# Optimization experiments

Measured on AMD Instinct MI355X. Metric: run time of the kernel, lower is better.

Reference implementation:

```python
import jax, jax.numpy as jnp
import numpy as np
from functools import partial

N_NODES = 50000
N_EDGES = 1600000
D_IN, D_HID, D_OUT = 128, 128, 64


def gcn_layer(h, src, dst, w, W, b, act):
    # linear
    h = h @ W.T + b  # [N, d_out]
    n = h.shape[0]
    # degree with self-loop: rowsum = 1 + sum_{e: src=i} w_e (coalesce is linear, so dup-sum is implicit)
    deg = 1.0 + jax.ops.segment_sum(w, src, num_segments=n)
    d_inv = jnp.where(deg > 0, deg ** -0.5, 0.0)  # deg >= 1 so never inf; matches torch isinf->0
    # normalized SpMM: self-loop term + neighbor aggregation
    ew = d_inv[src] * w * d_inv[dst]  # [E]
    agg = jax.ops.segment_sum(ew[:, None] * h[dst], src, num_segments=n)  # [N, d_out]
    out = (d_inv ** 2)[:, None] * h + agg
    if act:
        out = jax.nn.relu(out)
    return out


def setup_inputs() -> dict:
    key = jax.random.key(0)
    ks = jax.random.split(key, 9)
    x = jax.random.normal(ks[0], (N_NODES, D_IN), dtype=jnp.float32)
    edge_index = jax.random.randint(ks[1], (2, N_EDGES), 0, N_NODES, dtype=jnp.int64)
    edge_weight = jnp.ones((N_EDGES,), dtype=jnp.float32)
    def xavier(k, fan_out, fan_in, gain=jnp.sqrt(2.0)):
        std = gain * jnp.sqrt(2.0 / (fan_in + fan_out))
        return (std * jax.random.normal(k, (fan_out, fan_in))).astype(jnp.float32)
    W1 = xavier(ks[2], D_HID, D_IN); b1 = jnp.zeros((D_HID,), jnp.float32)
    W2 = xavier(ks[3], D_HID, D_HID); b2 = jnp.zeros((D_HID,), jnp.float32)
    W3 = xavier(ks[4], D_OUT, D_HID); b3 = jnp.zeros((D_OUT,), jnp.float32)
    return {"x": x, "edge_index": edge_index, "edge_weight": edge_weight,
            "W1": W1, "b1": b1, "W2": W2, "b2": b2, "W3": W3, "b3": b3}


def reference(x, edge_index, edge_weight, W1, b1, W2, b2, W3, b3):
    src, dst = edge_index[0], edge_index[1]
    h = gcn_layer(x, src, dst, edge_weight, W1, b1, act=True)
    h = gcn_layer(h, src, dst, edge_weight, W2, b2, act=True)
    h = gcn_layer(h, src, dst, edge_weight, W3, b3, act=False)
    return h
```

## Files before the change

kernel.cpp:

```cpp
#include <hip/hip_runtime.h>


#define THREADS 256
#define CAP 72

typedef unsigned short bfu;

static inline int ceil_div(int a, int b) { return (a + b - 1) / b; }
static inline size_t alignup(size_t x) { return (x + 255) & ~(size_t)255; }


__global__ void k_zero(int* __restrict__ flag) {
  if (threadIdx.x == 0 && blockIdx.x == 0) { flag[0] = 0; flag[1] = 0; }
}


__global__ void k_init(int* __restrict__ counts, int n,
                       const int* __restrict__ ei_words,
                       const float* __restrict__ w, int e,
                       int* __restrict__ flag) {
  int i = blockIdx.x * blockDim.x + threadIdx.x;
  if (i < n) counts[i] = 0;
  if (i == 0) {
    int is64 = 1;
    for (int k = 0; k < 64; ++k) {
      if (ei_words[2 * k + 1] != 0) { is64 = 0; break; }
    }
    if (is64) flag[0] = 1;
  }
  if (i < e) {
    if (w[i] != 1.0f) atomicExch(&flag[1], 1);
  }
}

__device__ __forceinline__ int load_idx(const void* base, long long i, int is64) {
  if (is64) return (int)((const long long*)base)[i];
  return ((const int*)base)[i];
}


__global__ void k_count(const void* __restrict__ ei, int* __restrict__ counts,
                        int e, const int* __restrict__ flag) {
  int i = blockIdx.x * blockDim.x + threadIdx.x;
  if (i < e) {
    int is64 = flag[0];
    int s = load_idx(ei, i, is64);
    atomicAdd(&counts[s], 1);
  }
}


#define SCAN_T 256
#define SCAN_ITEMS 8
#define SCAN_BLOCK (SCAN_T * SCAN_ITEMS)

__global__ void k_scan1(const int* __restrict__ counts, int* __restrict__ row_ptr1,
                        int* __restrict__ partials, int n) {
  __shared__ int sd[SCAN_T];
  int t = threadIdx.x;
  int base = blockIdx.x * SCAN_BLOCK + t * SCAN_ITEMS;
  int v[SCAN_ITEMS];
  int s = 0;
#pragma unroll
  for (int i = 0; i < SCAN_ITEMS; ++i) {
    int idx = base + i;
    v[i] = (idx < n) ? counts[idx] : 0;
    s += v[i];
  }
  sd[t] = s;
  __syncthreads();
  for (int off = 1; off < SCAN_T; off <<= 1) {
    int x = 0;
    if (t >= off) x = sd[t - off];
    __syncthreads();
    sd[t] += x;
    __syncthreads();
  }
  int run = (t > 0) ? sd[t - 1] : 0;
  if (t == SCAN_T - 1) partials[blockIdx.x] = sd[t];
#pragma unroll
  for (int i = 0; i < SCAN_ITEMS; ++i) {
    run += v[i];
    int idx = base + i;
    if (idx < n) row_ptr1[idx] = run;
  }
}

__global__ void k_scan2(int* __restrict__ partials, int nb) {
  if (blockIdx.x == 0 && threadIdx.x == 0) {
    int run = 0;
    for (int b = 0; b < nb; ++b) {
      int v = partials[b];
      partials[b] = run;
      run += v;
    }
  }
}

__global__ void k_scan3(int* __restrict__ row_ptr, const int* __restrict__ partials,
                        int* __restrict__ cursor, int n) {
  int i = blockIdx.x * blockDim.x + threadIdx.x;
  if (i < n) {
    int b = i / SCAN_BLOCK;
    int v = row_ptr[i + 1] + partials[b];
    row_ptr[i + 1] = v;
    if (i + 1 < n) cursor[i + 1] = v;
  }
  if (i == 0) { row_ptr[0] = 0; cursor[0] = 0; }
}


__global__ void k_fill(const void* __restrict__ ei, const float* __restrict__ w,
                       int* __restrict__ cur, int* __restrict__ eg, int e,
                       const int* __restrict__ flag, int use_ell) {
  int i = blockIdx.x * blockDim.x + threadIdx.x;
  if (i >= e) return;
  int is64 = flag[0];
  int wnot1 = flag[1];
  int s = load_idx(ei, i, is64);
  int d = load_idx(ei, (long long)e + i, is64);
  int r = atomicAdd(&cur[s], 1);
  int p;
  if (use_ell) {
    if (r >= CAP) return;
    p = s * CAP + r;
  } else {
    p = r;
  }
  if (wnot1) {
    ((int2*)eg)[p] = make_int2(d, __float_as_int(w[i]));
  } else {
    eg[p] = d;
  }
}


__global__ void k_deg_w1(const int* __restrict__ cnt, const int* __restrict__ rp,
                         float* __restrict__ dinv, int n,
                         const int* __restrict__ flag, int use_ell) {
  if (flag[1] != 0) return;
  int i = blockIdx.x * blockDim.x + threadIdx.x;
  if (i >= n) return;
  int len = use_ell ? min(cnt[i], CAP) : (rp[i + 1] - rp[i]);
  float d = 1.0f + (float)len;
  dinv[i] = 1.0f / sqrtf(d);
}


__global__ __launch_bounds__(256) void k_deg_gen(const int* __restrict__ eg,
                                                 const int* __restrict__ cnt,
                                                 const int* __restrict__ rp,
                                                 float* __restrict__ dinv, int n,
                                                 const int* __restrict__ flag,
                                                 int use_ell) {
  if (flag[1] == 0) return;
  constexpr int G = 16;
  int node = blockIdx.x * (256 / G) + threadIdx.x / G;
  int l = threadIdx.x & (G - 1);
  if (node >= n) return;
  const int2* eg2 = (const int2*)eg;
  int e0, e1;
  if (use_ell) { e0 = node * CAP; e1 = e0 + min(cnt[node], CAP); }
  else { e0 = rp[node]; e1 = rp[node + 1]; }
  float s = 0.f;
  for (int e = e0 + l; e < e1; e += G) s += __int_as_float(eg2[e].y);
  s += __shfl_xor(s, 8);
  s += __shfl_xor(s, 4);
  s += __shfl_xor(s, 2);
  s += __shfl_xor(s, 1);
  if (l == 0) {
    float d = 1.0f + s;
    dinv[node] = (d > 0.0f) ? (1.0f / sqrtf(d)) : 0.0f;
  }
}


__global__ __launch_bounds__(256) void k_scale(int* __restrict__ eg,
                                               const int* __restrict__ cnt,
                                               const int* __restrict__ rp,
                                               const float* __restrict__ dinv, int n,
                                               const int* __restrict__ flag,
                                               int use_ell) {
  if (flag[1] == 0) return;
  constexpr int G = 16;
  int node = blockIdx.x * (256 / G) + threadIdx.x / G;
  int l = threadIdx.x & (G - 1);
  if (node >= n) return;
  int2* eg2 = (int2*)eg;
  float ds = dinv[node];
  int e0, e1;
  if (use_ell) { e0 = node * CAP; e1 = e0 + min(cnt[node], CAP); }
  else { e0 = rp[node]; e1 = rp[node + 1]; }
  for (int e = e0 + l; e < e1; e += G) {
    int2 ed = eg2[e];
    float v = ds * __int_as_float(ed.y) * dinv[ed.x];
    eg2[e] = make_int2(ed.x, __float_as_int(v));
  }
}


__device__ __forceinline__ bfu f2bf(float f) {
  unsigned u = __float_as_uint(f);
  unsigned r = (u + 0x7fffu + ((u >> 16) & 1u)) >> 16;
  return (bfu)r;
}


__global__ __launch_bounds__(256) void k_gemm(const float* __restrict__ A,
                                              const float* __restrict__ W,
                                              const float* __restrict__ bias,
                                              bfu* __restrict__ O, int M, int Nc) {
  __shared__ float4 xs[64][17];
  __shared__ float4 wsm[64][17];
  int tid = threadIdx.x;
  int m0 = blockIdx.x * 64;
  int c0 = blockIdx.y * 64;
  int tx = tid & 15, ty = tid >> 4;

  const float4* A4 = (const float4*)A;
  const float4* W4 = (const float4*)W;

  int r0 = tid >> 4;
  int k40 = tid & 15;

  float acc[4][4];
#pragma unroll
  for (int i = 0; i < 4; ++i)
#pragma unroll
    for (int j = 0; j < 4; ++j) acc[i][j] = 0.f;

  for (int ks = 0; ks < 2; ++ks) {
    if (ks) __syncthreads();
#pragma unroll
    for (int f = 0; f < 4; ++f) {
      int r = r0 + 16 * f;
      int gr = m0 + r;
      xs[r][k40] = (gr < M) ? A4[(size_t)gr * 32 + ks * 16 + k40]
                            : make_float4(0.f, 0.f, 0.f, 0.f);
      int wr = c0 + r;
      wsm[r][k40] = (wr < Nc) ? W4[(size_t)wr * 32 + ks * 16 + k40]
                              : make_float4(0.f, 0.f, 0.f, 0.f);
    }
    __syncthreads();

#pragma unroll
    for (int k4 = 0; k4 < 16; ++k4) {
      float4 a[4], b[4];
#pragma unroll
      for (int i = 0; i < 4; ++i) a[i] = xs[ty + 16 * i][k4];
#pragma unroll
      for (int j = 0; j < 4; ++j) b[j] = wsm[tx + 16 * j][k4];
#pragma unroll
      for (int i = 0; i < 4; ++i)
#pragma unroll
        for (int j = 0; j < 4; ++j) {
          acc[i][j] = fmaf(a[i].x, b[j].x, acc[i][j]);
          acc[i][j] = fmaf(a[i].y, b[j].y, acc[i][j]);
          acc[i][j] = fmaf(a[i].z, b[j].z, acc[i][j]);
          acc[i][j] = fmaf(a[i].w, b[j].w, acc[i][j]);
        }
    }
  }

#pragma unroll
  for (int i = 0; i < 4; ++i) {
    int r = m0 + ty + 16 * i;
    if (r < M) {
#pragma unroll
      for (int j = 0; j < 4; ++j) {
        int c = c0 + tx + 16 * j;
        O[(size_t)r * Nc + c] = f2bf(acc[i][j] + bias[c]);
      }
    }
  }
}


#define FMA8(v, u, acc)                                                       \
  do {                                                                        \
    acc[0] = fmaf((v), __uint_as_float((u).x << 16), acc[0]);                 \
    acc[1] = fmaf((v), __uint_as_float((u).x & 0xffff0000u), acc[1]);         \
    acc[2] = fmaf((v), __uint_as_float((u).y << 16), acc[2]);                 \
    acc[3] = fmaf((v), __uint_as_float((u).y & 0xffff0000u), acc[3]);         \
    acc[4] = fmaf((v), __uint_as_float((u).z << 16), acc[4]);                 \
    acc[5] = fmaf((v), __uint_as_float((u).z & 0xffff0000u), acc[5]);         \
    acc[6] = fmaf((v), __uint_as_float((u).w << 16), acc[6]);                 \
    acc[7] = fmaf((v), __uint_as_float((u).w & 0xffff0000u), acc[7]);         \
  } while (0)

template <int D>
__global__ __launch_bounds__(256) void k_agg(const bfu* __restrict__ h,
                                             float* __restrict__ out,
                                             const int* __restrict__ rp,
                                             const int* __restrict__ cnt,
                                             const int* __restrict__ eg,
                                             const float* __restrict__ dinv, int n,
                                             int relu, int use_ell,
                                             const int* __restrict__ flag) {
  constexpr int TG = D / 8;
  constexpr int PER = 256 / TG;
  int node = blockIdx.x * PER + threadIdx.x / TG;
  int q = threadIdx.x & (TG - 1);
  if (node >= n) return;
  const uint4* h8 = (const uint4*)h;
  int wnot1 = flag[1];
  int e0, e1;
  if (use_ell) { e0 = node * CAP; e1 = e0 + min(cnt[node], CAP); }
  else { e0 = rp[node]; e1 = rp[node + 1]; }
  float di = dinv[node];
  float accA[8], accB[8];
#pragma unroll
  for (int k = 0; k < 8; ++k) { accA[k] = 0.f; accB[k] = 0.f; }
  int e = e0;
  if (!wnot1) {
    for (; e + 4 <= e1; e += 4) {
      int d0 = eg[e], d1 = eg[e + 1], d2 = eg[e + 2], d3 = eg[e + 3];
      float v0 = di * dinv[d0], v1 = di * dinv[d1];
      float v2 = di * dinv[d2], v3 = di * dinv[d3];
      uint4 u0 = h8[(size_t)d0 * TG + q];
      uint4 u1 = h8[(size_t)d1 * TG + q];
      uint4 u2 = h8[(size_t)d2 * TG + q];
      uint4 u3 = h8[(size_t)d3 * TG + q];
      FMA8(v0, u0, accA);
      FMA8(v1, u1, accB);
      FMA8(v2, u2, accA);
      FMA8(v3, u3, accB);
    }
    for (; e < e1; ++e) {
      int d = eg[e];
      float v = di * dinv[d];
      uint4 u = h8[(size_t)d * TG + q];
      FMA8(v, u, accB);
    }
  } else {
    const int2* eg2 = (const int2*)eg;
    for (; e + 4 <= e1; e += 4) {
      int2 E0 = eg2[e], E1 = eg2[e + 1], E2 = eg2[e + 2], E3 = eg2[e + 3];
      float v0 = __int_as_float(E0.y), v1 = __int_as_float(E1.y);
      float v2 = __int_as_float(E2.y), v3 = __int_as_float(E3.y);
      uint4 u0 = h8[(size_t)E0.x * TG + q];
      uint4 u1 = h8[(size_t)E1.x * TG + q];
      uint4 u2 = h8[(size_t)E2.x * TG + q];
      uint4 u3 = h8[(size_t)E3.x * TG + q];
      FMA8(v0, u0, accA);
      FMA8(v1, u1, accB);
      FMA8(v2, u2, accA);
      FMA8(v3, u3, accB);
    }
    for (; e < e1; ++e) {
      int2 ed = eg2[e];
      float v = __int_as_float(ed.y);
      uint4 u = h8[(size_t)ed.x * TG + q];
      FMA8(v, u, accB);
    }
  }
  float dd = di * di;
  uint4 us = h8[(size_t)node * TG + q];
  FMA8(dd, us, accA);
  float s[8];
#pragma unroll
  for (int k = 0; k < 8; ++k) {
    s[k] = accA[k] + accB[k];
    if (relu) s[k] = fmaxf(s[k], 0.f);
  }
  float4 o0 = make_float4(s[0], s[1], s[2], s[3]);
  float4 o1 = make_float4(s[4], s[5], s[6], s[7]);
  float4* orow = (float4*)out;
  orow[(size_t)node * (D / 4) + 2 * q] = o0;
  orow[(size_t)node * (D / 4) + 2 * q + 1] = o1;
}


extern "C" void kernel_launch(void* const* d_in, const int* in_sizes, int n_in,
                              void* d_out, int out_size, void* d_ws, size_t ws_size,
                              hipStream_t stream) {
  const float* x = (const float*)d_in[0];
  const void* edge_index = d_in[1];
  const float* ew = (const float*)d_in[2];
  const float* W1 = (const float*)d_in[3];
  const float* b1 = (const float*)d_in[4];
  const float* W2 = (const float*)d_in[5];
  const float* b2 = (const float*)d_in[6];
  const float* W3 = (const float*)d_in[7];
  const float* b3 = (const float*)d_in[8];

  const int N = in_sizes[0] / 128;
  const int E = in_sizes[2];

  size_t fixed = 256  + alignup((size_t)N * 4)
               + alignup((size_t)N * 4)  + alignup((size_t)(N + 1) * 4)
               + 256  + alignup((size_t)N * 128 * 2)
               + alignup((size_t)N * 128 * 4) ;
  size_t ell_bytes = alignup((size_t)N * CAP * 8);
  size_t csr_bytes = alignup((size_t)E * 8);
  int use_ell = (fixed + ell_bytes <= ws_size) ? 1 : 0;

  char* p = (char*)d_ws;
  auto alloc = [&](size_t bytes) {
    void* r = (void*)p;
    p += alignup(bytes);
    return r;
  };
  int* flag = (int*)alloc(8);
  float* dinv = (float*)alloc((size_t)N * 4);
  int* cnt = (int*)alloc((size_t)N * 4);
  int* rp = (int*)alloc((size_t)(N + 1) * 4);
  int* partials = (int*)alloc(64 * 4);
  int* eg = (int*)alloc(use_ell ? ell_bytes : csr_bytes);
  bfu* bufA = (bfu*)alloc((size_t)N * 128 * 2);
  float* bufB = (float*)alloc((size_t)N * 128 * 4);

  float* out = (float*)d_out;

  k_zero<<<1, 64, 0, stream>>>(flag);

  k_init<<<ceil_div(E, THREADS), THREADS, 0, stream>>>(cnt, N, (const int*)edge_index, ew, E, flag);

  if (!use_ell) {
    int nb = ceil_div(N, SCAN_BLOCK);
    k_count<<<ceil_div(E, THREADS), THREADS, 0, stream>>>(edge_index, cnt, E, flag);
    k_scan1<<<nb, SCAN_T, 0, stream>>>(cnt, rp + 1, partials, N);
    k_scan2<<<1, 64, 0, stream>>>(partials, nb);
    k_scan3<<<ceil_div(N, THREADS), THREADS, 0, stream>>>(rp, partials, cnt, N);
  }

  k_fill<<<ceil_div(E, THREADS), THREADS, 0, stream>>>(edge_index, ew, cnt, eg, E, flag, use_ell);

  k_deg_w1<<<ceil_div(N, THREADS), THREADS, 0, stream>>>(cnt, rp, dinv, N, flag, use_ell);
  k_deg_gen<<<ceil_div(N, 16), 256, 0, stream>>>(eg, cnt, rp, dinv, N, flag, use_ell);
  k_scale<<<ceil_div(N, 16), 256, 0, stream>>>(eg, cnt, rp, dinv, N, flag, use_ell);

  {
    dim3 g(ceil_div(N, 64), 2);
    k_gemm<<<g, 256, 0, stream>>>(x, W1, b1, bufA, N, 128);
    k_agg<128><<<ceil_div(N, 16), 256, 0, stream>>>(bufA, bufB, rp, cnt, eg, dinv, N, 1, use_ell, flag);
  }
  {
    dim3 g(ceil_div(N, 64), 2);
    k_gemm<<<g, 256, 0, stream>>>(bufB, W2, b2, bufA, N, 128);
    k_agg<128><<<ceil_div(N, 16), 256, 0, stream>>>(bufA, bufB, rp, cnt, eg, dinv, N, 1, use_ell, flag);
  }
  {
    dim3 g(ceil_div(N, 64), 1);
    k_gemm<<<g, 256, 0, stream>>>(bufB, W3, b3, bufA, N, 64);
    k_agg<64><<<ceil_div(N, 32), 256, 0, stream>>>(bufA, out, rp, cnt, eg, dinv, N, 0, use_ell, flag);
  }
}
```

Measured before the change: 454.5 us.

## Co-schedule first-layer GEMM with edge fill in one launch; unroll aggregation by 8

The first linear layer does not depend on the graph structure, so its GEMM blocks now run in the same launch as the edge-fill scatter, with block ids split between the two roles. The memory-bound, atomic-heavy fill and the compute-bound GEMM can then overlap and one launch disappears. The unweighted aggregation loop also now processes 8 neighbours per iteration and issues all row loads before the dinv loads, for more memory-level parallelism. In exchange, the fused kernel reserves GEMM-sized shared memory for the fill blocks too, which may lower their occupancy, and the wider unroll raises register pressure.

```diff
diff --git a/kernel.cpp b/kernel.cpp
--- a/kernel.cpp
+++ b/kernel.cpp
@@ -13,7 +13,6 @@
 __global__ void k_zero(int* __restrict__ flag) {
   if (threadIdx.x == 0 && blockIdx.x == 0) { flag[0] = 0; flag[1] = 0; }
 }
-
 
 __global__ void k_init(int* __restrict__ counts, int n,
                        const int* __restrict__ ei_words,
@@ -49,7 +48,6 @@
   }
 }
 
-
 #define SCAN_T 256
 #define SCAN_ITEMS 8
 #define SCAN_BLOCK (SCAN_T * SCAN_ITEMS)
@@ -110,27 +108,97 @@
 }
 
 
-__global__ void k_fill(const void* __restrict__ ei, const float* __restrict__ w,
-                       int* __restrict__ cur, int* __restrict__ eg, int e,
-                       const int* __restrict__ flag, int use_ell) {
-  int i = blockIdx.x * blockDim.x + threadIdx.x;
-  if (i >= e) return;
-  int is64 = flag[0];
-  int wnot1 = flag[1];
-  int s = load_idx(ei, i, is64);
-  int d = load_idx(ei, (long long)e + i, is64);
-  int r = atomicAdd(&cur[s], 1);
-  int p;
-  if (use_ell) {
-    if (r >= CAP) return;
-    p = s * CAP + r;
+__device__ __forceinline__ bfu f2bf(float f) {
+  unsigned u = __float_as_uint(f);
+  unsigned r = (u + 0x7fffu + ((u >> 16) & 1u)) >> 16;
+  return (bfu)r;
+}
+
+
+__global__ __launch_bounds__(256) void k_fill_gemm(
+    const float* __restrict__ A, const float* __restrict__ W,
+    const float* __restrict__ bias, bfu* __restrict__ O, int M, int gemm_blocks,
+    const void* __restrict__ ei, const float* __restrict__ w,
+    int* __restrict__ cur, int* __restrict__ eg, int e,
+    const int* __restrict__ flag, int use_ell) {
+  __shared__ float4 xs[64][17];
+  __shared__ float4 wsm[64][17];
+  int bid = blockIdx.x;
+  if (bid < gemm_blocks) {
+    const int Nc = 128;
+    int tid = threadIdx.x;
+    int m0 = (bid >> 1) * 64;
+    int c0 = (bid & 1) * 64;
+    int tx = tid & 15, ty = tid >> 4;
+    const float4* A4 = (const float4*)A;
+    const float4* W4 = (const float4*)W;
+    int r0 = tid >> 4;
+    int k40 = tid & 15;
+    float acc[4][4];
+#pragma unroll
+    for (int i = 0; i < 4; ++i)
+#pragma unroll
+      for (int j = 0; j < 4; ++j) acc[i][j] = 0.f;
+    for (int ks = 0; ks < 2; ++ks) {
+      if (ks) __syncthreads();
+#pragma unroll
+      for (int f = 0; f < 4; ++f) {
+        int r = r0 + 16 * f;
+        int gr = m0 + r;
+        xs[r][k40] = (gr < M) ? A4[(size_t)gr * 32 + ks * 16 + k40]
+                              : make_float4(0.f, 0.f, 0.f, 0.f);
+        wsm[r][k40] = W4[(size_t)(c0 + r) * 32 + ks * 16 + k40];
+      }
+      __syncthreads();
+#pragma unroll
+      for (int k4 = 0; k4 < 16; ++k4) {
+        float4 a[4], b[4];
+#pragma unroll
+        for (int i = 0; i < 4; ++i) a[i] = xs[ty + 16 * i][k4];
+#pragma unroll
+        for (int j = 0; j < 4; ++j) b[j] = wsm[tx + 16 * j][k4];
+#pragma unroll
+        for (int i = 0; i < 4; ++i)
+#pragma unroll
+          for (int j = 0; j < 4; ++j) {
+            acc[i][j] = fmaf(a[i].x, b[j].x, acc[i][j]);
+            acc[i][j] = fmaf(a[i].y, b[j].y, acc[i][j]);
+            acc[i][j] = fmaf(a[i].z, b[j].z, acc[i][j]);
+            acc[i][j] = fmaf(a[i].w, b[j].w, acc[i][j]);
+          }
+      }
+    }
+#pragma unroll
+    for (int i = 0; i < 4; ++i) {
+      int r = m0 + ty + 16 * i;
+      if (r < M) {
+#pragma unroll
+        for (int j = 0; j < 4; ++j) {
+          int c = c0 + tx + 16 * j;
+          O[(size_t)r * Nc + c] = f2bf(acc[i][j] + bias[c]);
+        }
+      }
+    }
   } else {
-    p = r;
-  }
-  if (wnot1) {
-    ((int2*)eg)[p] = make_int2(d, __float_as_int(w[i]));
-  } else {
-    eg[p] = d;
+    int i = (bid - gemm_blocks) * blockDim.x + threadIdx.x;
+    if (i >= e) return;
+    int is64 = flag[0];
+    int wnot1 = flag[1];
+    int s = load_idx(ei, i, is64);
+    int d = load_idx(ei, (long long)e + i, is64);
+    int r = atomicAdd(&cur[s], 1);
+    int p;
+    if (use_ell) {
+      if (r >= CAP) return;
+      p = s * CAP + r;
+    } else {
+      p = r;
+    }
+    if (wnot1) {
+      ((int2*)eg)[p] = make_int2(d, __float_as_int(w[i]));
+    } else {
+      eg[p] = d;
+    }
   }
 }
 
@@ -145,7 +213,6 @@
   float d = 1.0f + (float)len;
   dinv[i] = 1.0f / sqrtf(d);
 }
-
 
 __global__ __launch_bounds__(256) void k_deg_gen(const int* __restrict__ eg,
                                                  const int* __restrict__ cnt,
@@ -174,7 +241,6 @@
   }
 }
 
-
 __global__ __launch_bounds__(256) void k_scale(int* __restrict__ eg,
                                                const int* __restrict__ cnt,
                                                const int* __restrict__ rp,
@@ -196,13 +262,6 @@
     float v = ds * __int_as_float(ed.y) * dinv[ed.x];
     eg2[e] = make_int2(ed.x, __float_as_int(v));
   }
-}
-
-
-__device__ __forceinline__ bfu f2bf(float f) {
-  unsigned u = __float_as_uint(f);
-  unsigned r = (u + 0x7fffu + ((u >> 16) & 1u)) >> 16;
-  return (bfu)r;
 }
 
 
@@ -313,14 +372,38 @@
   for (int k = 0; k < 8; ++k) { accA[k] = 0.f; accB[k] = 0.f; }
   int e = e0;
   if (!wnot1) {
-    for (; e + 4 <= e1; e += 4) {
+    for (; e + 8 <= e1; e += 8) {
       int d0 = eg[e], d1 = eg[e + 1], d2 = eg[e + 2], d3 = eg[e + 3];
-      float v0 = di * dinv[d0], v1 = di * dinv[d1];
-      float v2 = di * dinv[d2], v3 = di * dinv[d3];
+      int d4 = eg[e + 4], d5 = eg[e + 5], d6 = eg[e + 6], d7 = eg[e + 7];
       uint4 u0 = h8[(size_t)d0 * TG + q];
       uint4 u1 = h8[(size_t)d1 * TG + q];
       uint4 u2 = h8[(size_t)d2 * TG + q];
       uint4 u3 = h8[(size_t)d3 * TG + q];
+      uint4 u4 = h8[(size_t)d4 * TG + q];
+      uint4 u5 = h8[(size_t)d5 * TG + q];
+      uint4 u6 = h8[(size_t)d6 * TG + q];
+      uint4 u7 = h8[(size_t)d7 * TG + q];
+      float v0 = di * dinv[d0], v1 = di * dinv[d1];
+      float v2 = di * dinv[d2], v3 = di * dinv[d3];
+      float v4 = di * dinv[d4], v5 = di * dinv[d5];
+      float v6 = di * dinv[d6], v7 = di * dinv[d7];
+      FMA8(v0, u0, accA);
+      FMA8(v1, u1, accB);
+      FMA8(v2, u2, accA);
+      FMA8(v3, u3, accB);
+      FMA8(v4, u4, accA);
+      FMA8(v5, u5, accB);
+      FMA8(v6, u6, accA);
+      FMA8(v7, u7, accB);
+    }
+    for (; e + 4 <= e1; e += 4) {
+      int d0 = eg[e], d1 = eg[e + 1], d2 = eg[e + 2], d3 = eg[e + 3];
+      uint4 u0 = h8[(size_t)d0 * TG + q];
+      uint4 u1 = h8[(size_t)d1 * TG + q];
+      uint4 u2 = h8[(size_t)d2 * TG + q];
+      uint4 u3 = h8[(size_t)d3 * TG + q];
+      float v0 = di * dinv[d0], v1 = di * dinv[d1];
+      float v2 = di * dinv[d2], v3 = di * dinv[d3];
       FMA8(v0, u0, accA);
       FMA8(v1, u1, accB);
       FMA8(v2, u2, accA);
@@ -413,7 +496,6 @@
   float* out = (float*)d_out;
 
   k_zero<<<1, 64, 0, stream>>>(flag);
-
   k_init<<<ceil_div(E, THREADS), THREADS, 0, stream>>>(cnt, N, (const int*)edge_index, ew, E, flag);
 
   if (!use_ell) {
@@ -424,17 +506,18 @@
     k_scan3<<<ceil_div(N, THREADS), THREADS, 0, stream>>>(rp, partials, cnt, N);
   }
 
-  k_fill<<<ceil_div(E, THREADS), THREADS, 0, stream>>>(edge_index, ew, cnt, eg, E, flag, use_ell);
+  {
+    int gemm_blocks = ceil_div(N, 64) * 2;
+    int fill_blocks = ceil_div(E, THREADS);
+    k_fill_gemm<<<gemm_blocks + fill_blocks, THREADS, 0, stream>>>(
+        x, W1, b1, bufA, N, gemm_blocks, edge_index, ew, cnt, eg, E, flag, use_ell);
+  }
 
   k_deg_w1<<<ceil_div(N, THREADS), THREADS, 0, stream>>>(cnt, rp, dinv, N, flag, use_ell);
   k_deg_gen<<<ceil_div(N, 16), 256, 0, stream>>>(eg, cnt, rp, dinv, N, flag, use_ell);
   k_scale<<<ceil_div(N, 16), 256, 0, stream>>>(eg, cnt, rp, dinv, N, flag, use_ell);
 
-  {
-    dim3 g(ceil_div(N, 64), 2);
-    k_gemm<<<g, 256, 0, stream>>>(x, W1, b1, bufA, N, 128);
-    k_agg<128><<<ceil_div(N, 16), 256, 0, stream>>>(bufA, bufB, rp, cnt, eg, dinv, N, 1, use_ell, flag);
-  }
+  k_agg<128><<<ceil_div(N, 16), 256, 0, stream>>>(bufA, bufB, rp, cnt, eg, dinv, N, 1, use_ell, flag);
   {
     dim3 g(ceil_div(N, 64), 2);
     k_gemm<<<g, 256, 0, stream>>>(bufB, W2, b2, bufA, N, 128);
```

Result: no change. 448.2 us (-1.4%).
